# Kernel optimization log

Measured on AMD Instinct MI355X. Metric: run time of the kernel, lower is better.

Reference implementation:

```python
import jax, jax.numpy as jnp
import numpy as np

OUT_H = OUT_W = 7
SAMPLE = 2          # sample_num (sampling_ratio)
SCALE = 0.125       # spatial_scale
IMG = 1600.0        # image size implied by scale * feature size


def setup_inputs() -> dict:
    key = jax.random.key(0)
    k1, k2, k3, k4 = jax.random.split(key, 4)
    N, C, H, W = 2, 256, 200, 200
    K = 1000
    features = jax.random.normal(k1, (N, C, H, W), dtype=jnp.float32)
    b = jax.random.randint(k2, (K,), 0, N).astype(jnp.float32)
    xy = jax.random.uniform(k3, (K, 4), dtype=jnp.float32) * IMG  # raw corners
    x1 = jnp.minimum(xy[:, 0], xy[:, 2]); x2 = jnp.maximum(xy[:, 0], xy[:, 2])
    y1 = jnp.minimum(xy[:, 1], xy[:, 3]); y2 = jnp.maximum(xy[:, 1], xy[:, 3])
    rois = jnp.stack([b, x1, y1, x2, y2], axis=1)  # [K,5]
    return {"features": features, "rois": rois}


def _roi_align(features, rois):
    # Faithful port of torchvision roi_align (aligned=False, sampling_ratio=SAMPLE)
    N, C, H, W = features.shape
    K = rois.shape[0]
    b = rois[:, 0].astype(jnp.int32)
    x1 = rois[:, 1] * SCALE; y1 = rois[:, 2] * SCALE
    x2 = rois[:, 3] * SCALE; y2 = rois[:, 4] * SCALE
    roi_w = jnp.maximum(x2 - x1, 1.0)  # aligned=False forces min size 1
    roi_h = jnp.maximum(y2 - y1, 1.0)
    bin_w = roi_w / OUT_W
    bin_h = roi_h / OUT_H

    # sample coordinates: [K, out*S] along each axis
    pbin = jnp.repeat(jnp.arange(OUT_H, dtype=jnp.float32), SAMPLE)      # bin index
    sub = jnp.tile(jnp.arange(SAMPLE, dtype=jnp.float32) + 0.5, OUT_H)   # sub-sample offset
    ys = y1[:, None] + pbin[None] * bin_h[:, None] + sub[None] * bin_h[:, None] / SAMPLE  # [K,Ny]
    xs = x1[:, None] + pbin[None] * bin_w[:, None] + sub[None] * bin_w[:, None] / SAMPLE  # [K,Nx]

    def axis_terms(c, size):
        valid = (c >= -1.0) & (c <= size)        # torch: zero outside [-1, size]
        c = jnp.maximum(c, 0.0)
        lo0 = jnp.floor(c).astype(jnp.int32)
        hi_edge = lo0 >= size - 1
        lo = jnp.where(hi_edge, size - 1, lo0)
        hi = jnp.where(hi_edge, size - 1, lo0 + 1)
        c = jnp.where(hi_edge, jnp.float32(size - 1), c)
        l = c - lo.astype(jnp.float32)           # fractional part
        return valid, lo, hi, l

    vy, yl, yh, ly = axis_terms(ys, H)
    vx, xl, xh, lx = axis_terms(xs, W)
    hy, hx = 1.0 - ly, 1.0 - lx

    def gather(yi, xi):
        # [K,Ny,Nx,C] gather with per-roi batch index
        return features[b[:, None, None], :, yi[:, :, None], xi[:, None, :]]

    val = (hy[:, :, None] * hx[:, None, :])[..., None] * gather(yl, xl) \
        + (hy[:, :, None] * lx[:, None, :])[..., None] * gather(yl, xh) \
        + (ly[:, :, None] * hx[:, None, :])[..., None] * gather(yh, xl) \
        + (ly[:, :, None] * lx[:, None, :])[..., None] * gather(yh, xh)
    mask = (vy[:, :, None] & vx[:, None, :])[..., None]
    val = jnp.where(mask, val, 0.0)

    # average SAMPLE x SAMPLE points per bin -> [K,C,OUT_H,OUT_W]
    val = val.reshape(K, OUT_H, SAMPLE, OUT_W, SAMPLE, C).mean(axis=(2, 4))
    return val.transpose(0, 3, 1, 2)


def reference(features, rois):
    return _roi_align(features, rois)
```

## Files before the change

kernel.cpp:

```cpp
#include <hip/hip_runtime.h>

constexpr int C = 256, H = 200, W = 200, NB = 2;
constexpr int PH = 7, PW = 7;
constexpr int NS = 14;
constexpr float SCALE = 0.125f;
constexpr int CG = 32, NCG = C / CG;
constexpr int CGF = 8, NGROUPF = C / CGF;

typedef float f32x4 __attribute__((ext_vector_type(4)));

__global__ __launch_bounds__(256) void transpose_kernel(
    const float* __restrict__ feat, ushort* __restrict__ T)
{
    __shared__ float tile[32][36];
    int B = blockIdx.x;
    int xt = B % 7; int tmp = B / 7;
    int y  = tmp % H; tmp /= H;
    int nb = tmp & 1; int cg = tmp >> 1;
    int x0 = xt * 32;
    int xw = min(32, W - x0);

    int t = threadIdx.x;
    {
        int cl = t >> 3, xi = (t & 7) * 4;
        if (xi < xw) {
            const float* src = feat + (((size_t)nb * C + cg * CG + cl) * H + y) * W + x0 + xi;
            float4 v = *reinterpret_cast<const float4*>(src);
            tile[xi + 0][cl] = v.x; tile[xi + 1][cl] = v.y;
            tile[xi + 2][cl] = v.z; tile[xi + 3][cl] = v.w;
        }
    }
    __syncthreads();
    int xl = t >> 3, c4 = (t & 7) * 4;
    if (xl < xw) {
        float4 v = *reinterpret_cast<const float4*>(&tile[xl][c4]);
        uint u0 = __float_as_uint(v.x), u1 = __float_as_uint(v.y);
        uint u2 = __float_as_uint(v.z), u3 = __float_as_uint(v.w);
        u0 = (u0 + 0x7FFFu + ((u0 >> 16) & 1u)) >> 16;
        u1 = (u1 + 0x7FFFu + ((u1 >> 16) & 1u)) >> 16;
        u2 = (u2 + 0x7FFFu + ((u2 >> 16) & 1u)) >> 16;
        u3 = (u3 + 0x7FFFu + ((u3 >> 16) & 1u)) >> 16;
        uint2 o; o.x = u0 | (u1 << 16); o.y = u2 | (u3 << 16);
        ushort* dst = T + ((((size_t)cg * NB + nb) * H + y) * W + (x0 + xl)) * CG + c4;
        *reinterpret_cast<uint2*>(dst) = o;
    }
}

__global__ __launch_bounds__(256) void gather_kernel(
    const ushort* __restrict__ T, const float* __restrict__ rois,
    float* __restrict__ out, int K)
{
    __shared__ int   s_ylo[NS], s_yhi[NS], s_xlo[NS], s_xhi[NS];
    __shared__ float s_wy[NS][2], s_wx[NS][2];
    __shared__ int   s_off[PH * PW * 16];
    __shared__ float s_wgt[PH * PW * 16];
    __shared__ float s_out[CG * PH * PW];

    int B  = blockIdx.x;
    int cg = B & 7;
    int j  = B >> 3;
    int p  = j / K, k = j - p * K;

    const float* r = rois + (size_t)k * 5;
    int b = (int)r[0];
    if (b != p) return;

    float x1 = r[1]*SCALE, y1 = r[2]*SCALE, x2 = r[3]*SCALE, y2 = r[4]*SCALE;
    float bw = fmaxf(x2 - x1, 1.0f) * (1.0f / PW);
    float bh = fmaxf(y2 - y1, 1.0f) * (1.0f / PH);

    int t = threadIdx.x;
    if (t < NS) {
        int ph = t >> 1, s = t & 1;
        float y = y1 + (float)ph * bh + ((float)s + 0.5f) * bh * 0.5f;
        bool v = (y >= -1.0f) && (y <= (float)H);
        float yc = fmaxf(y, 0.0f);
        int lo = (int)yc, hi;
        if (lo >= H - 1) { lo = H - 1; hi = H - 1; yc = (float)(H - 1); }
        else             { hi = lo + 1; }
        float l = yc - (float)lo;
        s_ylo[t] = lo; s_yhi[t] = hi;
        s_wy[t][0] = v ? 1.0f - l : 0.0f;
        s_wy[t][1] = v ? l        : 0.0f;
    } else if (t >= 64 && t < 64 + NS) {
        int i = t - 64, pw = i >> 1, s = i & 1;
        float x = x1 + (float)pw * bw + ((float)s + 0.5f) * bw * 0.5f;
        bool v = (x >= -1.0f) && (x <= (float)W);
        float xc = fmaxf(x, 0.0f);
        int lo = (int)xc, hi;
        if (lo >= W - 1) { lo = W - 1; hi = W - 1; xc = (float)(W - 1); }
        else             { hi = lo + 1; }
        float l = xc - (float)lo;
        s_xlo[i] = lo; s_xhi[i] = hi;
        s_wx[i][0] = v ? 1.0f - l : 0.0f;
        s_wx[i][1] = v ? l        : 0.0f;
    }
    __syncthreads();

    for (int i = t; i < PH * PW * 16; i += 256) {
        int bin = i >> 4, cr = i & 15;
        int ph = bin / PW, pw = bin - ph * PW;
        int sy = cr >> 3, sx = (cr >> 2) & 1, cy = (cr >> 1) & 1, cx = cr & 1;
        int ysi = 2 * ph + sy, xsi = 2 * pw + sx;
        int row = cy ? s_yhi[ysi] : s_ylo[ysi];
        int col = cx ? s_xhi[xsi] : s_xlo[xsi];
        s_off[i] = (row * W + col) * CG;
        s_wgt[i] = s_wy[ysi][cy] * s_wx[xsi][cx] * 0.25f;
    }
    __syncthreads();

    if (t < PH * PW * 4) {
        int bin = t >> 2, q = t & 3;
        const ushort* slab = T + ((size_t)(cg * NB + p) * H * W) * CG + q * 8;
        const int*   po = s_off + bin * 16;
        const float* pg = s_wgt + bin * 16;
        float a0=0,a1=0,a2=0,a3=0,a4=0,a5=0,a6=0,a7=0;
        #pragma unroll
        for (int cr = 0; cr < 16; ++cr) {
            int off = po[cr]; float w = pg[cr];
            const uint4 d = *reinterpret_cast<const uint4*>(slab + off);
            a0 += w * __uint_as_float(d.x << 16);
            a1 += w * __uint_as_float(d.x & 0xFFFF0000u);
            a2 += w * __uint_as_float(d.y << 16);
            a3 += w * __uint_as_float(d.y & 0xFFFF0000u);
            a4 += w * __uint_as_float(d.z << 16);
            a5 += w * __uint_as_float(d.z & 0xFFFF0000u);
            a6 += w * __uint_as_float(d.w << 16);
            a7 += w * __uint_as_float(d.w & 0xFFFF0000u);
        }
        float* so = s_out + (8 * q) * (PH * PW) + bin;
        so[0*49]=a0; so[1*49]=a1; so[2*49]=a2; so[3*49]=a3;
        so[4*49]=a4; so[5*49]=a5; so[6*49]=a6; so[7*49]=a7;
    }
    __syncthreads();

    float* oslab = out + ((size_t)k * C + cg * CG) * (PH * PW);
    for (int i4 = t; i4 < (CG * PH * PW) / 4; i4 += 256) {
        f32x4 v = *reinterpret_cast<const f32x4*>(s_out + 4 * i4);
        __builtin_nontemporal_store(v, reinterpret_cast<f32x4*>(oslab + 4 * i4));
    }
}

struct __attribute__((packed, aligned(4))) f2 { float a, b; };

__global__ __launch_bounds__(256) void roi_align_fallback(
    const float* __restrict__ feat, const float* __restrict__ rois,
    float* __restrict__ out, int K)
{
    __shared__ int   s_ylo[NS], s_yhi[NS];
    __shared__ float s_wy[NS][2];
    __shared__ int   s_xb[NS];
    __shared__ float s_wx[NS][2];

    int B   = blockIdx.x;
    int xcd = B & 7;
    int j   = B >> 3;
    int p   = j / K, k = j - p * K;
    int cb  = (p * 8 + xcd) * CGF;

    const float* r = rois + (size_t)k * 5;
    int   b  = (int)r[0];
    float x1 = r[1]*SCALE, y1 = r[2]*SCALE, x2 = r[3]*SCALE, y2 = r[4]*SCALE;
    float bw = fmaxf(x2 - x1, 1.0f) * (1.0f / PW);
    float bh = fmaxf(y2 - y1, 1.0f) * (1.0f / PH);

    int t = threadIdx.x;
    if (t < NS) {
        int ph = t >> 1, s = t & 1;
        float y = y1 + (float)ph * bh + ((float)s + 0.5f) * bh * 0.5f;
        bool v = (y >= -1.0f) && (y <= (float)H);
        float yc = fmaxf(y, 0.0f);
        int lo = (int)yc, hi;
        if (lo >= H - 1) { lo = H - 1; hi = H - 1; yc = (float)(H - 1); }
        else             { hi = lo + 1; }
        float l = yc - (float)lo;
        s_ylo[t] = lo; s_yhi[t] = hi;
        s_wy[t][0] = v ? 1.0f - l : 0.0f;
        s_wy[t][1] = v ? l        : 0.0f;
    } else if (t >= 64 && t < 64 + NS) {
        int i = t - 64, pw = i >> 1, s = i & 1;
        float x = x1 + (float)pw * bw + ((float)s + 0.5f) * bw * 0.5f;
        bool v = (x >= -1.0f) && (x <= (float)W);
        float xc = fmaxf(x, 0.0f);
        int lo = (int)xc;
        if (lo >= W - 1) {
            s_xb[i] = W - 2; s_wx[i][0] = 0.0f; s_wx[i][1] = v ? 1.0f : 0.0f;
        } else {
            float l = xc - (float)lo;
            s_xb[i] = lo; s_wx[i][0] = v ? 1.0f - l : 0.0f; s_wx[i][1] = v ? l : 0.0f;
        }
    }
    __syncthreads();

    const float* img = feat + (size_t)b * (C * H * W);
    float* out_base = out + ((size_t)k * C + cb) * (PH * PW);

    for (int i = t; i < CGF * PH * PW; i += 256) {
        int cl  = i / (PH * PW);
        int bin = i - cl * (PH * PW);
        int ph  = bin / PW;
        int pw  = bin - ph * PW;
        const float* plane = img + (size_t)(cb + cl) * (H * W);

        float acc = 0.0f;
        #pragma unroll
        for (int sy = 0; sy < 2; ++sy) {
            int ysi = 2 * ph + sy;
            const float* rlo = plane + s_ylo[ysi] * W;
            const float* rhi = plane + s_yhi[ysi] * W;
            float hy = s_wy[ysi][0], ly = s_wy[ysi][1];
            #pragma unroll
            for (int sx = 0; sx < 2; ++sx) {
                int xsi = 2 * pw + sx;
                int xb = s_xb[xsi];
                float w0 = s_wx[xsi][0], w1 = s_wx[xsi][1];
                f2 vlo = *reinterpret_cast<const f2*>(rlo + xb);
                f2 vhi = *reinterpret_cast<const f2*>(rhi + xb);
                acc += hy * (w0 * vlo.a + w1 * vlo.b)
                     + ly * (w0 * vhi.a + w1 * vhi.b);
            }
        }
        __builtin_nontemporal_store(acc * 0.25f, &out_base[i]);
    }
}

extern "C" void kernel_launch(void* const* d_in, const int* in_sizes, int n_in,
                              void* d_out, int out_size, void* d_ws, size_t ws_size,
                              hipStream_t stream) {
    const float* feat = (const float*)d_in[0];
    const float* rois = (const float*)d_in[1];
    float* out = (float*)d_out;
    int K = in_sizes[1] / 5;

    size_t need = (size_t)NCG * NB * H * W * CG * sizeof(ushort);
    if (ws_size >= need) {
        ushort* T = (ushort*)d_ws;
        int tblocks = NCG * NB * H * 7;
        transpose_kernel<<<tblocks, 256, 0, stream>>>(feat, T);
        gather_kernel<<<K * NCG * NB, 256, 0, stream>>>(T, rois, out, K);
    } else {
        roi_align_fallback<<<K * NGROUPF, 256, 0, stream>>>(feat, rois, out, K);
    }
}
```

Measured before the change: 58.67 us.

## Tile transpose over four rows and inline sample-coordinate math in gather

The transpose kernel now handles four feature rows per block, which cuts the block count by four and gives each thread more independent loads. Its bf16 workspace writes become nontemporal stores. The gather kernel drops the separate per-axis coordinate pass and one barrier: each thread recomputes its own sample coordinates and weights, and the offset/weight tables are padded to stride 17. The aim is lower launch and barrier overhead, paid for with redundant arithmetic and a larger shared-memory tile.

```diff
diff --git a/kernel.cpp b/kernel.cpp
--- a/kernel.cpp
+++ b/kernel.cpp
@@ -5,44 +5,52 @@
 constexpr int NS = 14;
 constexpr float SCALE = 0.125f;
 constexpr int CG = 32, NCG = C / CG;
+constexpr int TY = 4;
 constexpr int CGF = 8, NGROUPF = C / CGF;
 
 typedef float f32x4 __attribute__((ext_vector_type(4)));
+typedef uint  u32x2 __attribute__((ext_vector_type(2)));
 
 __global__ __launch_bounds__(256) void transpose_kernel(
     const float* __restrict__ feat, ushort* __restrict__ T)
 {
-    __shared__ float tile[32][36];
+    __shared__ float tile[TY][32][36];
     int B = blockIdx.x;
     int xt = B % 7; int tmp = B / 7;
-    int y  = tmp % H; tmp /= H;
+    int yt = tmp % (H / TY); tmp /= (H / TY);
     int nb = tmp & 1; int cg = tmp >> 1;
-    int x0 = xt * 32;
+    int x0 = xt * 32, y0 = yt * TY;
     int xw = min(32, W - x0);
 
     int t = threadIdx.x;
     {
         int cl = t >> 3, xi = (t & 7) * 4;
         if (xi < xw) {
-            const float* src = feat + (((size_t)nb * C + cg * CG + cl) * H + y) * W + x0 + xi;
-            float4 v = *reinterpret_cast<const float4*>(src);
-            tile[xi + 0][cl] = v.x; tile[xi + 1][cl] = v.y;
-            tile[xi + 2][cl] = v.z; tile[xi + 3][cl] = v.w;
+            const float* src = feat + (((size_t)nb * C + cg * CG + cl) * H + y0) * W + x0 + xi;
+            #pragma unroll
+            for (int yy = 0; yy < TY; ++yy) {
+                float4 v = *reinterpret_cast<const float4*>(src + yy * W);
+                tile[yy][xi + 0][cl] = v.x; tile[yy][xi + 1][cl] = v.y;
+                tile[yy][xi + 2][cl] = v.z; tile[yy][xi + 3][cl] = v.w;
+            }
         }
     }
     __syncthreads();
     int xl = t >> 3, c4 = (t & 7) * 4;
     if (xl < xw) {
-        float4 v = *reinterpret_cast<const float4*>(&tile[xl][c4]);
-        uint u0 = __float_as_uint(v.x), u1 = __float_as_uint(v.y);
-        uint u2 = __float_as_uint(v.z), u3 = __float_as_uint(v.w);
-        u0 = (u0 + 0x7FFFu + ((u0 >> 16) & 1u)) >> 16;
-        u1 = (u1 + 0x7FFFu + ((u1 >> 16) & 1u)) >> 16;
-        u2 = (u2 + 0x7FFFu + ((u2 >> 16) & 1u)) >> 16;
-        u3 = (u3 + 0x7FFFu + ((u3 >> 16) & 1u)) >> 16;
-        uint2 o; o.x = u0 | (u1 << 16); o.y = u2 | (u3 << 16);
-        ushort* dst = T + ((((size_t)cg * NB + nb) * H + y) * W + (x0 + xl)) * CG + c4;
-        *reinterpret_cast<uint2*>(dst) = o;
+        #pragma unroll
+        for (int yy = 0; yy < TY; ++yy) {
+            float4 v = *reinterpret_cast<const float4*>(&tile[yy][xl][c4]);
+            uint u0 = __float_as_uint(v.x), u1 = __float_as_uint(v.y);
+            uint u2 = __float_as_uint(v.z), u3 = __float_as_uint(v.w);
+            u0 = (u0 + 0x7FFFu + ((u0 >> 16) & 1u)) >> 16;
+            u1 = (u1 + 0x7FFFu + ((u1 >> 16) & 1u)) >> 16;
+            u2 = (u2 + 0x7FFFu + ((u2 >> 16) & 1u)) >> 16;
+            u3 = (u3 + 0x7FFFu + ((u3 >> 16) & 1u)) >> 16;
+            u32x2 o; o.x = u0 | (u1 << 16); o.y = u2 | (u3 << 16);
+            ushort* dst = T + ((((size_t)cg * NB + nb) * H + (y0 + yy)) * W + (x0 + xl)) * CG + c4;
+            __builtin_nontemporal_store(o, reinterpret_cast<u32x2*>(dst));
+        }
     }
 }
 
@@ -50,11 +58,9 @@
     const ushort* __restrict__ T, const float* __restrict__ rois,
     float* __restrict__ out, int K)
 {
-    __shared__ int   s_ylo[NS], s_yhi[NS], s_xlo[NS], s_xhi[NS];
-    __shared__ float s_wy[NS][2], s_wx[NS][2];
-    __shared__ int   s_off[PH * PW * 16];
-    __shared__ float s_wgt[PH * PW * 16];
-    __shared__ float s_out[CG * PH * PW];
+    __shared__ int   s_off[49 * 17];
+    __shared__ float s_wgt[49 * 17];
+    __shared__ float s_out[CG * 49];
 
     int B  = blockIdx.x;
     int cg = B & 7;
@@ -70,50 +76,39 @@
     float bh = fmaxf(y2 - y1, 1.0f) * (1.0f / PH);
 
     int t = threadIdx.x;
-    if (t < NS) {
-        int ph = t >> 1, s = t & 1;
-        float y = y1 + (float)ph * bh + ((float)s + 0.5f) * bh * 0.5f;
-        bool v = (y >= -1.0f) && (y <= (float)H);
-        float yc = fmaxf(y, 0.0f);
-        int lo = (int)yc, hi;
-        if (lo >= H - 1) { lo = H - 1; hi = H - 1; yc = (float)(H - 1); }
-        else             { hi = lo + 1; }
-        float l = yc - (float)lo;
-        s_ylo[t] = lo; s_yhi[t] = hi;
-        s_wy[t][0] = v ? 1.0f - l : 0.0f;
-        s_wy[t][1] = v ? l        : 0.0f;
-    } else if (t >= 64 && t < 64 + NS) {
-        int i = t - 64, pw = i >> 1, s = i & 1;
-        float x = x1 + (float)pw * bw + ((float)s + 0.5f) * bw * 0.5f;
-        bool v = (x >= -1.0f) && (x <= (float)W);
-        float xc = fmaxf(x, 0.0f);
-        int lo = (int)xc, hi;
-        if (lo >= W - 1) { lo = W - 1; hi = W - 1; xc = (float)(W - 1); }
-        else             { hi = lo + 1; }
-        float l = xc - (float)lo;
-        s_xlo[i] = lo; s_xhi[i] = hi;
-        s_wx[i][0] = v ? 1.0f - l : 0.0f;
-        s_wx[i][1] = v ? l        : 0.0f;
-    }
-    __syncthreads();
-
-    for (int i = t; i < PH * PW * 16; i += 256) {
+    for (int i = t; i < 49 * 16; i += 256) {
         int bin = i >> 4, cr = i & 15;
-        int ph = bin / PW, pw = bin - ph * PW;
-        int sy = cr >> 3, sx = (cr >> 2) & 1, cy = (cr >> 1) & 1, cx = cr & 1;
-        int ysi = 2 * ph + sy, xsi = 2 * pw + sx;
-        int row = cy ? s_yhi[ysi] : s_ylo[ysi];
-        int col = cx ? s_xhi[xsi] : s_xlo[xsi];
-        s_off[i] = (row * W + col) * CG;
-        s_wgt[i] = s_wy[ysi][cy] * s_wx[xsi][cx] * 0.25f;
-    }
-    __syncthreads();
-
-    if (t < PH * PW * 4) {
+        int ph = bin / 7, pw = bin - ph * 7;
+        int sy = (cr >> 3) & 1, sx = (cr >> 2) & 1, cy = (cr >> 1) & 1, cx = cr & 1;
+
+        float ys = y1 + (float)ph * bh + ((float)sy + 0.5f) * bh * 0.5f;
+        bool vy = (ys >= -1.0f) && (ys <= (float)H);
+        float yc = fmaxf(ys, 0.0f);
+        int ylo = (int)yc, yhi; float lyv;
+        if (ylo >= H - 1) { ylo = H - 1; yhi = H - 1; lyv = 0.0f; }
+        else              { yhi = ylo + 1; lyv = yc - (float)ylo; }
+        int   row = cy ? yhi : ylo;
+        float wy  = vy ? (cy ? lyv : 1.0f - lyv) : 0.0f;
+
+        float xs = x1 + (float)pw * bw + ((float)sx + 0.5f) * bw * 0.5f;
+        bool vx = (xs >= -1.0f) && (xs <= (float)W);
+        float xc = fmaxf(xs, 0.0f);
+        int xlo = (int)xc, xhi; float lxv;
+        if (xlo >= W - 1) { xlo = W - 1; xhi = W - 1; lxv = 0.0f; }
+        else              { xhi = xlo + 1; lxv = xc - (float)xlo; }
+        int   col = cx ? xhi : xlo;
+        float wx  = vx ? (cx ? lxv : 1.0f - lxv) : 0.0f;
+
+        s_off[bin * 17 + cr] = (row * W + col) * CG;
+        s_wgt[bin * 17 + cr] = wy * wx * 0.25f;
+    }
+    __syncthreads();
+
+    if (t < 49 * 4) {
         int bin = t >> 2, q = t & 3;
         const ushort* slab = T + ((size_t)(cg * NB + p) * H * W) * CG + q * 8;
-        const int*   po = s_off + bin * 16;
-        const float* pg = s_wgt + bin * 16;
+        const int*   po = s_off + bin * 17;
+        const float* pg = s_wgt + bin * 17;
         float a0=0,a1=0,a2=0,a3=0,a4=0,a5=0,a6=0,a7=0;
         #pragma unroll
         for (int cr = 0; cr < 16; ++cr) {
@@ -128,14 +123,14 @@
             a6 += w * __uint_as_float(d.w << 16);
             a7 += w * __uint_as_float(d.w & 0xFFFF0000u);
         }
-        float* so = s_out + (8 * q) * (PH * PW) + bin;
+        float* so = s_out + (8 * q) * 49 + bin;
         so[0*49]=a0; so[1*49]=a1; so[2*49]=a2; so[3*49]=a3;
         so[4*49]=a4; so[5*49]=a5; so[6*49]=a6; so[7*49]=a7;
     }
     __syncthreads();
 
     float* oslab = out + ((size_t)k * C + cg * CG) * (PH * PW);
-    for (int i4 = t; i4 < (CG * PH * PW) / 4; i4 += 256) {
+    for (int i4 = t; i4 < (CG * 49) / 4; i4 += 256) {
         f32x4 v = *reinterpret_cast<const f32x4*>(s_out + 4 * i4);
         __builtin_nontemporal_store(v, reinterpret_cast<f32x4*>(oslab + 4 * i4));
     }
@@ -235,7 +230,7 @@
     size_t need = (size_t)NCG * NB * H * W * CG * sizeof(ushort);
     if (ws_size >= need) {
         ushort* T = (ushort*)d_ws;
-        int tblocks = NCG * NB * H * 7;
+        int tblocks = NCG * NB * (H / TY) * 7;
         transpose_kernel<<<tblocks, 256, 0, stream>>>(feat, T);
         gather_kernel<<<K * NCG * NB, 256, 0, stream>>>(T, rois, out, K);
     } else {
```

Result: slower. 72.09 us (+22.9%).
